# Kernel tuning notes

Measured on AMD Instinct MI355X. Metric: run time of the kernel, lower is better.

The kernel has to match this reference:

```python
import jax, jax.numpy as jnp
import numpy as np

N = 30000       # nodes
E = 480000      # edges (before self loops)
IN = 128        # in_channels
H1, C1 = 5, 64  # conv1 heads, per-head channels
OUT = 64        # out_channels (conv2, heads=1)
PE = 100000     # pos/neg edges for decode
NEG_SLOPE = 0.2


def setup_inputs() -> dict:
    key = jax.random.key(0)
    ks = jax.random.split(key, 12)
    return {
        "x": jax.random.normal(ks[0], (N, IN), dtype=jnp.float32),
        "edge_index": jax.random.randint(ks[1], (2, E), 0, N),
        "pos_edge_index": jax.random.randint(ks[2], (2, PE), 0, N),
        "neg_edge_index": jax.random.randint(ks[3], (2, PE), 0, N),
        "W1": jax.random.normal(ks[4], (IN, H1 * C1), dtype=jnp.float32) * 0.05,
        "att_src1": jax.random.normal(ks[5], (H1, C1), dtype=jnp.float32) * 0.1,
        "att_dst1": jax.random.normal(ks[6], (H1, C1), dtype=jnp.float32) * 0.1,
        "b1": jnp.zeros((H1 * C1,), dtype=jnp.float32),
        "W2": jax.random.normal(ks[7], (H1 * C1, OUT), dtype=jnp.float32) * 0.05,
        "att_src2": jax.random.normal(ks[8], (1, OUT), dtype=jnp.float32) * 0.1,
        "att_dst2": jax.random.normal(ks[9], (1, OUT), dtype=jnp.float32) * 0.1,
        "b2": jnp.zeros((OUT,), dtype=jnp.float32),
    }


def gat_conv(x, edge_index, W, att_src, att_dst, bias, heads, out_ch):
    """PyG GATConv: add self loops, linear proj, edge softmax, scatter-sum, concat heads."""
    n = x.shape[0]
    loops = jnp.arange(n)
    src = jnp.concatenate([edge_index[0], loops])  # message sources j
    dst = jnp.concatenate([edge_index[1], loops])  # message targets i
    h = (x @ W).reshape(n, heads, out_ch)          # [N,H,C]
    a_src = jnp.sum(h * att_src, axis=-1)          # [N,H]
    a_dst = jnp.sum(h * att_dst, axis=-1)          # [N,H]
    e = jax.nn.leaky_relu(a_src[src] + a_dst[dst], NEG_SLOPE)  # [E',H]
    # numerically-stable segment softmax over incoming edges of each dst node
    m = jax.ops.segment_max(e, dst, num_segments=n)
    m = jax.lax.stop_gradient(jnp.where(jnp.isfinite(m), m, 0.0))
    ex = jnp.exp(e - m[dst])
    s = jax.ops.segment_sum(ex, dst, num_segments=n)
    alpha = ex / (s[dst] + 1e-16)                  # [E',H]
    out = jax.ops.segment_sum(alpha[:, :, None] * h[src], dst, num_segments=n)  # [N,H,C]
    return out.reshape(n, heads * out_ch) + bias


def reference(x, edge_index, pos_edge_index, neg_edge_index,
              W1, att_src1, att_dst1, b1, W2, att_src2, att_dst2, b2):
    z = gat_conv(x, edge_index, W1, att_src1, att_dst1, b1, H1, C1)
    z = jax.nn.relu(z)
    z = gat_conv(z, edge_index, W2, att_src2, att_dst2, b2, 1, OUT)
    ei = jnp.concatenate([pos_edge_index, neg_edge_index], axis=-1)
    return jnp.sum(z[ei[0]] * z[ei[1]], axis=-1)  # [2*PE]
```

## Files before the change

### kernel.cpp

```cpp
#include <hip/hip_runtime.h>
#include <hip/hip_fp16.h>
#include <cstdint>
#include <cstddef>
#include <type_traits>

#define N_NODES 30000
#define N_EDGES 480000
#define N_EDGES_SL (N_EDGES + N_NODES)
#define IN_CH 128
#define HEADS1 5
#define C1 64
#define D1 (HEADS1 * C1)
#define OUT_CH 64
#define PE_CNT 100000
#define NEG_SLOPE 0.2f
#define BCAP 64
#define GEMM1_BLOCKS 469
#define INIT_BLOCKS 120
#define BB 120
#define EPB (N_EDGES / BB)
#define NW (N_NODES / 2)
#define PFX_BLOCKS 59
#define OVF_CAP 65536

typedef _Float16 f16x8 __attribute__((ext_vector_type(8)));
typedef _Float16 f16x2 __attribute__((ext_vector_type(2)));
typedef float fx4 __attribute__((ext_vector_type(4)));

#if defined(__has_builtin)
#if __has_builtin(__builtin_amdgcn_fdot2)
#define HAS_FDOT2 1
#endif
#endif

static __device__ __forceinline__ float leaky(float x) {
    return fmaxf(x, NEG_SLOPE * x);
}

template<int NH, int SP, typename AT>
static __device__ __forceinline__ void gemm_phase(const AT* __restrict__ A,
                                                  const __half* __restrict__ Wt,
                                                  __half* __restrict__ C, int K,
                                                  const float* __restrict__ att_src,
                                                  const float* __restrict__ att_dst,
                                                  float* __restrict__ as_out,
                                                  float* __restrict__ ad_out,
                                                  int slot, int nsl, int lane) {
    const int N = NH * 64;
    int q = lane >> 4, l16 = lane & 15;
    for (int tile = slot; tile < N_NODES / 16; tile += nsl) {
        int rowBase = tile * 16;
        int arow = rowBase + l16;
        fx4 zero4 = {0.f, 0.f, 0.f, 0.f};
        fx4 acc[NH][4];
#pragma unroll
        for (int h = 0; h < NH; ++h)
#pragma unroll
            for (int c = 0; c < 4; ++c) acc[h][c] = zero4;
        for (int kk = 0; kk < K; kk += 32) {
            f16x8 af;
            if constexpr (std::is_same<AT, float>::value) {
                const float4* s = (const float4*)(A + (size_t)arow * K + kk + q * 8);
                float4 v0 = s[0], v1 = s[1];
                af[0] = (_Float16)v0.x; af[1] = (_Float16)v0.y;
                af[2] = (_Float16)v0.z; af[3] = (_Float16)v0.w;
                af[4] = (_Float16)v1.x; af[5] = (_Float16)v1.y;
                af[6] = (_Float16)v1.z; af[7] = (_Float16)v1.w;
            } else {
                af = *(const f16x8*)((const __half*)A + (size_t)arow * K + kk + q * 8);
            }
#pragma unroll
            for (int h = 0; h < NH; ++h) {
#pragma unroll
                for (int c = 0; c < 4; ++c) {
                    int col = h * 64 + c * 16 + l16;
                    f16x8 bf = *(const f16x8*)(Wt + (size_t)col * K + kk + q * 8);
                    acc[h][c] = __builtin_amdgcn_mfma_f32_16x16x32_f16(af, bf, acc[h][c], 0, 0, 0);
                }
            }
        }
#pragma unroll
        for (int h = 0; h < NH; ++h) {
            float ps[4] = {0.f, 0.f, 0.f, 0.f};
            float pd[4] = {0.f, 0.f, 0.f, 0.f};
#pragma unroll
            for (int c = 0; c < 4; ++c) {
                int gcol = h * 64 + c * 16 + l16;
                float av = att_src[gcol];
                float dv = att_dst[gcol];
#pragma unroll
                for (int reg = 0; reg < 4; ++reg) {
                    int grow = rowBase + q * 4 + reg;
                    float val = acc[h][c][reg];
                    C[(size_t)grow * N + gcol] = __float2half(val);
                    ps[reg] += val * av;
                    pd[reg] += val * dv;
                }
            }
#pragma unroll
            for (int off = 1; off < 16; off <<= 1) {
#pragma unroll
                for (int reg = 0; reg < 4; ++reg) {
                    ps[reg] += __shfl_xor(ps[reg], off, 64);
                    pd[reg] += __shfl_xor(pd[reg], off, 64);
                }
            }
            if (l16 == 0) {
#pragma unroll
                for (int reg = 0; reg < 4; ++reg) {
                    int grow = rowBase + q * 4 + reg;
                    as_out[(size_t)grow * SP + h] = ps[reg];
                    ad_out[(size_t)grow * SP + h] = pd[reg];
                }
            }
        }
    }
}

__global__ __launch_bounds__(512) void k_init(int* __restrict__ ovfc,
                                              int* __restrict__ esrc2,
                                              const float* __restrict__ W1,
                                              __half* __restrict__ Wt1,
                                              const float* __restrict__ W2,
                                              __half* __restrict__ Wt2,
                                              const int* __restrict__ edge,
                                              unsigned* __restrict__ partA) {
    __shared__ unsigned bins[NW];
    if (blockIdx.x < INIT_BLOCKS) {
        int t = blockIdx.x * 512 + threadIdx.x;
        int nthr = INIT_BLOCKS * 512;
        for (int i = t; i < N_NODES; i += nthr) esrc2[i * BCAP] = i;
        if (t == 0) *ovfc = 0;
        const int T1 = IN_CH * D1, T2 = D1 * OUT_CH;
        for (int idx = t; idx < T1 + T2; idx += nthr) {
            if (idx < T1) {
                int k = idx / D1, n = idx - k * D1;
                Wt1[(size_t)n * IN_CH + k] = __float2half(W1[idx]);
            } else {
                int i2 = idx - T1;
                int k = i2 / OUT_CH, n = i2 - k * OUT_CH;
                Wt2[(size_t)n * D1 + k] = __float2half(W2[i2]);
            }
        }
    } else {
        int b = blockIdx.x - INIT_BLOCKS;
        for (int i = threadIdx.x; i < NW; i += 512) bins[i] = 0;
        __syncthreads();
        int e0 = b * EPB;
        for (int e = e0 + ((int)threadIdx.x << 2); e < e0 + EPB; e += 2048) {
            int4 dd = *(const int4*)(edge + N_EDGES + e);
            atomicAdd(&bins[dd.x >> 1], (dd.x & 1) ? 65536u : 1u);
            atomicAdd(&bins[dd.y >> 1], (dd.y & 1) ? 65536u : 1u);
            atomicAdd(&bins[dd.z >> 1], (dd.z & 1) ? 65536u : 1u);
            atomicAdd(&bins[dd.w >> 1], (dd.w & 1) ? 65536u : 1u);
        }
        __syncthreads();
        for (int i = threadIdx.x; i < NW; i += 512)
            partA[(size_t)b * NW + i] = bins[i];
    }
}

__global__ __launch_bounds__(256) void k_build_gemm1(const unsigned* __restrict__ partA,
                                                     unsigned* __restrict__ offA,
                                                     int* __restrict__ cnt,
                                                     const float* __restrict__ x,
                                                     const __half* __restrict__ Wt1,
                                                     __half* __restrict__ h1,
                                                     const float* __restrict__ att_src1,
                                                     const float* __restrict__ att_dst1,
                                                     float* __restrict__ as1,
                                                     float* __restrict__ ad1) {
    int lane = threadIdx.x & 63, wv = threadIdx.x >> 6;
    if (blockIdx.x < GEMM1_BLOCKS) {
        gemm_phase<HEADS1, 8, float>(x, Wt1, h1, IN_CH, att_src1, att_dst1, as1, ad1,
                                     blockIdx.x * 4 + wv, GEMM1_BLOCKS * 4, lane);
    } else {
        int w = (blockIdx.x - GEMM1_BLOCKS) * 256 + threadIdx.x;
        if (w < NW) {
            unsigned s0 = 1, s1 = 1;
            for (int b0 = 0; b0 < BB; b0 += 10) {
                unsigned v[10];
#pragma unroll
                for (int u = 0; u < 10; ++u)
                    v[u] = partA[(size_t)(b0 + u) * NW + w];
#pragma unroll
                for (int u = 0; u < 10; ++u) {
                    offA[(size_t)(b0 + u) * NW + w] = min(s0, 64u) | (min(s1, 64u) << 16);
                    s0 += v[u] & 0xFFFFu;
                    s1 += v[u] >> 16;
                }
            }
            cnt[2 * w] = (int)s0;
            cnt[2 * w + 1] = (int)s1;
        }
    }
}

__global__ __launch_bounds__(512) void k_rank(const int* __restrict__ edge,
                                              const unsigned* __restrict__ offA,
                                              int* __restrict__ esrc2,
                                              int* __restrict__ ovf_cnt,
                                              int* __restrict__ ovf) {
    __shared__ unsigned bins[NW];
    int b = blockIdx.x;
    for (int i = threadIdx.x; i < NW; i += 512) bins[i] = 0;
    __syncthreads();
    int e0 = b * EPB;
    for (int e = e0 + ((int)threadIdx.x << 2); e < e0 + EPB; e += 2048) {
        int4 dd = *(const int4*)(edge + N_EDGES + e);
        int4 ss = *(const int4*)(edge + e);
        int dv[4] = {dd.x, dd.y, dd.z, dd.w};
        int sv[4] = {ss.x, ss.y, ss.z, ss.w};
#pragma unroll
        for (int u = 0; u < 4; ++u) {
            int d = dv[u];
            unsigned ret = atomicAdd(&bins[d >> 1], (d & 1) ? 65536u : 1u);
            unsigned lr = (d & 1) ? (ret >> 16) : (ret & 0xFFFFu);
            unsigned off = offA[(size_t)b * NW + (d >> 1)];
            off = (d & 1) ? (off >> 16) : (off & 0xFFFFu);
            unsigned slot = off + lr;
            if (slot < BCAP) {
                esrc2[(d << 6) + slot] = sv[u];
            } else {
                int oi = atomicAdd(ovf_cnt, 1);
                if (oi < OVF_CAP) { ovf[2 * oi] = d; ovf[2 * oi + 1] = sv[u]; }
            }
        }
    }
}

template<int NH, int NS, bool RELU>
static __device__ __forceinline__ void gather_all(const __half* __restrict__ base,
                                                  const unsigned (&wpkw)[NH][64],
                                                  const int (&jbufw)[64],
                                                  float (&redw)[584],
                                                  const float* __restrict__ bias,
                                                  __half* __restrict__ zrow,
                                                  int es, int cg, int lane) {
    int kA = es, kB = es + 8, kC = es + 16, kD = es + 24;
    int jA = jbufw[kA], jB = jbufw[kB];
    int jC = (NS == 4) ? jbufw[kC] : 0;
    int jD = (NS == 4) ? jbufw[kD] : 0;
    float4 v[NH][4];
#pragma unroll
    for (int h = 0; h < NH; ++h) {
        const __half* hb = base + h * 64;
        v[h][0] = *(const float4*)(hb + jA);
        v[h][1] = *(const float4*)(hb + jB);
        if (NS == 4) {
            v[h][2] = *(const float4*)(hb + jC);
            v[h][3] = *(const float4*)(hb + jD);
        }
    }
#pragma unroll
    for (int h = 0; h < NH; ++h) {
        unsigned uA = wpkw[h][kA], uB = wpkw[h][kB];
        __half2 hwA = *(__half2*)&uA, hwB = *(__half2*)&uB;
        const __half2* pA = (const __half2*)&v[h][0];
        const __half2* pB = (const __half2*)&v[h][1];
        __half2 a2[4] = {__half2{0, 0}, __half2{0, 0}, __half2{0, 0}, __half2{0, 0}};
#pragma unroll
        for (int i = 0; i < 4; ++i) {
            a2[i] = __hfma2(pA[i], hwA, a2[i]);
            a2[i] = __hfma2(pB[i], hwB, a2[i]);
        }
        if (NS == 4) {
            unsigned uC = wpkw[h][kC], uD = wpkw[h][kD];
            __half2 hwC = *(__half2*)&uC, hwD = *(__half2*)&uD;
            const __half2* pC = (const __half2*)&v[h][2];
            const __half2* pD = (const __half2*)&v[h][3];
#pragma unroll
            for (int i = 0; i < 4; ++i) {
                a2[i] = __hfma2(pC[i], hwC, a2[i]);
                a2[i] = __hfma2(pD[i], hwD, a2[i]);
            }
        }
#pragma unroll
        for (int i = 0; i < 4; ++i) {
            float2 f = __half22float2(a2[i]);
            redw[(cg * 8 + 2 * i) * 9 + es] = f.x;
            redw[(cg * 8 + 2 * i + 1) * 9 + es] = f.y;
        }
        float tot = 0.f;
#pragma unroll
        for (int e2 = 0; e2 < 8; ++e2)
            tot += redw[lane * 9 + e2];
        float o = tot + bias[h * 64 + lane];
        if (RELU) o = fmaxf(o, 0.f);
        zrow[h * 64 + lane] = __float2half(o);
    }
}

template<int NH, bool RELU>
__global__ __launch_bounds__(256) void k_attn_agg(const int* __restrict__ cnt,
                                                  const int* __restrict__ esrc2,
                                                  const int* __restrict__ ovf_cnt,
                                                  const int* __restrict__ ovf,
                                                  const __half* __restrict__ hf,
                                                  const float* __restrict__ a_src,
                                                  const float* __restrict__ a_dst,
                                                  const float* __restrict__ bias,
                                                  __half* __restrict__ zout) {
    const int SP = (NH == 1) ? 1 : 8;
    __shared__ unsigned wpk[4][NH][64];
    __shared__ int jbuf[4][64];
    __shared__ float red[4][584];
    int node = (blockIdx.x * 256 + threadIdx.x) >> 6;
    int lane = threadIdx.x & 63;
    int wv = threadIdx.x >> 6;
    if (node >= N_NODES) return;
    int deg = cnt[node];
    const int RS = NH * 64;
    float da[NH];
    if constexpr (NH == 1) {
        da[0] = a_dst[node];
    } else {
        float4 d0 = *(const float4*)(a_dst + (size_t)node * SP);
        da[0] = d0.x; da[1] = d0.y; da[2] = d0.z; da[3] = d0.w;
        da[4] = a_dst[(size_t)node * SP + 4];
    }
    if (deg <= BCAP) {
        int es = lane >> 3, cg = lane & 7;
        int joff = 0;
        float e[NH];
#pragma unroll
        for (int h = 0; h < NH; ++h) e[h] = 0.f;
        if (lane < deg) {
            int j = esrc2[node * BCAP + lane];
            joff = j * RS;
            if constexpr (NH == 1) {
                e[0] = __expf(leaky(a_src[j] + da[0]));
            } else {
                float4 s0 = *(const float4*)(a_src + (size_t)j * SP);
                float s4 = a_src[(size_t)j * SP + 4];
                e[0] = __expf(leaky(s0.x + da[0]));
                e[1] = __expf(leaky(s0.y + da[1]));
                e[2] = __expf(leaky(s0.z + da[2]));
                e[3] = __expf(leaky(s0.w + da[3]));
                e[4] = __expf(leaky(s4 + da[4]));
            }
        }
        float s[NH];
#pragma unroll
        for (int h = 0; h < NH; ++h) s[h] = e[h];
#pragma unroll
        for (int off = 1; off < 64; off <<= 1) {
#pragma unroll
            for (int h = 0; h < NH; ++h) s[h] += __shfl_xor(s[h], off, 64);
        }
#pragma unroll
        for (int h = 0; h < NH; ++h) {
            float r = 1.f / (s[h] + 1e-16f);
            __half2 wn = __float2half2_rn(e[h] * r);
            wpk[wv][h][lane] = *(unsigned*)&wn;
        }
        jbuf[wv][lane] = joff;
        const __half* base = hf + cg * 8;
        __half* zrow = zout + (size_t)node * RS;
        if (deg <= 16) {
            gather_all<NH, 2, RELU>(base, wpk[wv], jbuf[wv], red[wv], bias, zrow, es, cg, lane);
        } else if (deg <= 32) {
            gather_all<NH, 4, RELU>(base, wpk[wv], jbuf[wv], red[wv], bias, zrow, es, cg, lane);
        } else {
#pragma unroll
            for (int h = 0; h < NH; ++h) {
                const __half* hbase = hf + h * 64 + cg * 8;
                __half2 acch[4] = {__half2{0, 0}, __half2{0, 0}, __half2{0, 0}, __half2{0, 0}};
                for (int k0 = 0; k0 < deg; k0 += 32) {
                    int kA = k0 + es, kB = kA + 8, kC = kA + 16, kD = kA + 24;
                    unsigned uA = wpk[wv][h][kA];
                    unsigned uB = wpk[wv][h][kB];
                    unsigned uC = wpk[wv][h][kC];
                    unsigned uD = wpk[wv][h][kD];
                    int jA = jbuf[wv][kA];
                    int jB = jbuf[wv][kB];
                    int jC = jbuf[wv][kC];
                    int jD = jbuf[wv][kD];
                    float4 vA = *(const float4*)(hbase + jA);
                    float4 vB = *(const float4*)(hbase + jB);
                    float4 vC = *(const float4*)(hbase + jC);
                    float4 vD = *(const float4*)(hbase + jD);
                    __half2 hwA = *(__half2*)&uA, hwB = *(__half2*)&uB;
                    __half2 hwC = *(__half2*)&uC, hwD = *(__half2*)&uD;
                    const __half2* pA = (const __half2*)&vA;
                    const __half2* pB = (const __half2*)&vB;
                    const __half2* pC = (const __half2*)&vC;
                    const __half2* pD = (const __half2*)&vD;
#pragma unroll
                    for (int i = 0; i < 4; ++i) {
                        acch[i] = __hfma2(pA[i], hwA, acch[i]);
                        acch[i] = __hfma2(pB[i], hwB, acch[i]);
                        acch[i] = __hfma2(pC[i], hwC, acch[i]);
                        acch[i] = __hfma2(pD[i], hwD, acch[i]);
                    }
                }
#pragma unroll
                for (int i = 0; i < 4; ++i) {
                    float2 f = __half22float2(acch[i]);
                    red[wv][(cg * 8 + 2 * i) * 9 + es] = f.x;
                    red[wv][(cg * 8 + 2 * i + 1) * 9 + es] = f.y;
                }
                float tot = 0.f;
#pragma unroll
                for (int e2 = 0; e2 < 8; ++e2)
                    tot += red[wv][lane * 9 + e2];
                float o = tot + bias[h * 64 + lane];
                if (RELU) o = fmaxf(o, 0.f);
                zrow[h * 64 + lane] = __float2half(o);
            }
        }
    } else {
        int ovn = min(*ovf_cnt, OVF_CAP);
#pragma unroll
        for (int h = 0; h < NH; ++h) {
            float adsth = da[h];
            float sden = __expf(leaky(a_src[(size_t)esrc2[node * BCAP + lane] * SP + h] + adsth));
#pragma unroll
            for (int off = 1; off < 64; off <<= 1)
                sden += __shfl_xor(sden, off, 64);
            float s2 = 0.f;
            for (int k = lane; k < ovn; k += 64)
                if (ovf[2 * k] == node)
                    s2 += __expf(leaky(a_src[(size_t)ovf[2 * k + 1] * SP + h] + adsth));
#pragma unroll
            for (int off = 1; off < 64; off <<= 1)
                s2 += __shfl_xor(s2, off, 64);
            float r = 1.f / (sden + s2 + 1e-16f);
            float a = 0.f;
            for (int k = 0; k < BCAP; ++k) {
                int j = esrc2[node * BCAP + k];
                float w = __expf(leaky(a_src[(size_t)j * SP + h] + adsth));
                a += w * __half2float(hf[(size_t)j * RS + h * 64 + lane]);
            }
            for (int k = 0; k < ovn; ++k) {
                if (ovf[2 * k] == node) {
                    int j = ovf[2 * k + 1];
                    float w = __expf(leaky(a_src[(size_t)j * SP + h] + adsth));
                    a += w * __half2float(hf[(size_t)j * RS + h * 64 + lane]);
                }
            }
            float o = a * r + bias[h * 64 + lane];
            if (RELU) o = fmaxf(o, 0.f);
            zout[(size_t)node * RS + h * 64 + lane] = __float2half(o);
        }
    }
}

__global__ __launch_bounds__(256) void k_gemm2(const __half* __restrict__ z1,
                                               const __half* __restrict__ Wt2,
                                               __half* __restrict__ h2,
                                               const float* __restrict__ att_src2,
                                               const float* __restrict__ att_dst2,
                                               float* __restrict__ as2,
                                               float* __restrict__ ad2) {
    int lane = threadIdx.x & 63, wv = threadIdx.x >> 6;
    gemm_phase<1, 1, __half>(z1, Wt2, h2, D1, att_src2, att_dst2, as2, ad2,
                             blockIdx.x * 4 + wv, gridDim.x * 4, lane);
}

__global__ __launch_bounds__(256) void k_decode(const int* __restrict__ pos,
                                                const int* __restrict__ neg,
                                                const __half* __restrict__ z2,
                                                float* __restrict__ out) {
    int t = blockIdx.x * 256 + threadIdx.x;
    int e = t >> 3;
    int lc = t & 7;
    if (e >= 2 * PE_CNT) return;
    int a, b;
    if (e < PE_CNT) { a = pos[e]; b = pos[PE_CNT + e]; }
    else { int k = e - PE_CNT; a = neg[k]; b = neg[PE_CNT + k]; }
    union U { float4 f; f16x2 h[4]; __half2 hh[4]; } ua, ub;
    ua.f = *(const float4*)(z2 + (size_t)a * OUT_CH + lc * 8);
    ub.f = *(const float4*)(z2 + (size_t)b * OUT_CH + lc * 8);
    float v = 0.f;
#pragma unroll
    for (int i = 0; i < 4; ++i) {
#ifdef HAS_FDOT2
        v = __builtin_amdgcn_fdot2(ua.h[i], ub.h[i], v, false);
#else
        float2 fa = __half22float2(ua.hh[i]);
        float2 fb = __half22float2(ub.hh[i]);
        v += fa.x * fb.x + fa.y * fb.y;
#endif
    }
#pragma unroll
    for (int off = 1; off < 8; off <<= 1)
        v += __shfl_xor(v, off, 64);
    if (lc == 0) out[e] = v;
}

extern "C" void kernel_launch(void* const* d_in, const int* in_sizes, int n_in,
                              void* d_out, int out_size, void* d_ws, size_t ws_size,
                              hipStream_t stream) {
    const float* x        = (const float*)d_in[0];
    const int* edge_index = (const int*)d_in[1];
    const int* pos_ei     = (const int*)d_in[2];
    const int* neg_ei     = (const int*)d_in[3];
    const float* W1       = (const float*)d_in[4];
    const float* att_src1 = (const float*)d_in[5];
    const float* att_dst1 = (const float*)d_in[6];
    const float* b1       = (const float*)d_in[7];
    const float* W2       = (const float*)d_in[8];
    const float* att_src2 = (const float*)d_in[9];
    const float* att_dst2 = (const float*)d_in[10];
    const float* b2       = (const float*)d_in[11];
    float* out            = (float*)d_out;

    char* ws = (char*)d_ws;
    size_t off = 0;
    auto alloc = [&](size_t bytes) -> void* {
        void* p = ws + off;
        off = (off + bytes + 255) & ~(size_t)255;
        return p;
    };
    int* cnt     = (int*)alloc(sizeof(int) * N_NODES);
    int* ovfc    = (int*)alloc(sizeof(int) * 8);
    int* esrc2   = (int*)alloc(sizeof(int) * (size_t)N_NODES * BCAP);
    int* ovf     = (int*)alloc(sizeof(int) * (size_t)2 * OVF_CAP);
    __half* h1   = (__half*)alloc(sizeof(__half) * (size_t)N_NODES * D1);
    __half* z1   = (__half*)alloc(sizeof(__half) * (size_t)N_NODES * D1);
    __half* h2   = (__half*)alloc(sizeof(__half) * (size_t)N_NODES * OUT_CH);
    __half* z2   = (__half*)alloc(sizeof(__half) * (size_t)N_NODES * OUT_CH);
    __half* Wt1  = (__half*)alloc(sizeof(__half) * (size_t)D1 * IN_CH);
    __half* Wt2  = (__half*)alloc(sizeof(__half) * (size_t)OUT_CH * D1);
    float* as1   = (float*)alloc(sizeof(float) * (size_t)N_NODES * 8);
    float* ad1   = (float*)alloc(sizeof(float) * (size_t)N_NODES * 8);
    float* as2   = (float*)alloc(sizeof(float) * (size_t)N_NODES);
    float* ad2   = (float*)alloc(sizeof(float) * (size_t)N_NODES);
    unsigned* partA = (unsigned*)z1;
    unsigned* offA  = (unsigned*)((char*)z1 + (size_t)BB * NW * sizeof(unsigned));

    k_init<<<INIT_BLOCKS + BB, 512, 0, stream>>>(ovfc, esrc2, W1, Wt1, W2, Wt2,
                                                 edge_index, partA);
    k_build_gemm1<<<GEMM1_BLOCKS + PFX_BLOCKS, 256, 0, stream>>>(
        partA, offA, cnt, x, Wt1, h1, att_src1, att_dst1, as1, ad1);
    k_rank<<<BB, 512, 0, stream>>>(edge_index, offA, esrc2, ovfc, ovf);
    k_attn_agg<HEADS1, true><<<(N_NODES + 3) / 4, 256, 0, stream>>>(
        cnt, esrc2, ovfc, ovf, h1, as1, ad1, b1, z1);
    k_gemm2<<<469, 256, 0, stream>>>(z1, Wt2, h2, att_src2, att_dst2, as2, ad2);
    k_attn_agg<1, false><<<(N_NODES + 3) / 4, 256, 0, stream>>>(
        cnt, esrc2, ovfc, ovf, h2, as2, ad2, b2, z2);
    k_decode<<<(2 * PE_CNT * 8 + 255) / 256, 256, 0, stream>>>(pos_ei, neg_ei, z2, out);

    (void)in_sizes; (void)n_in; (void)out_size; (void)ws_size;
}
```

Measured before the change: 205.3 us.

## Fold attention projections into GEMM weights as extra MFMA column group

Precomputes W·att_src and W·att_dst as extra weight columns appended to the transposed fp16 weight matrices, so each GEMM computes the attention logits a_src/a_dst with one additional 16-column MFMA tile instead of a post-GEMM dot product plus cross-lane shuffle reduction. This removes the epilogue reductions and shuffles in both GEMMs. It also adds a launch bound hint of 2 waves-per-EU occupancy on the aggregation kernel. The logits are now computed from fp16-rounded folded weights, which changes numerics slightly.

```diff
diff --git a/kernel.cpp b/kernel.cpp
--- a/kernel.cpp
+++ b/kernel.cpp
@@ -11,7 +11,9 @@
 #define HEADS1 5
 #define C1 64
 #define D1 (HEADS1 * C1)
+#define D1X (D1 + 16)
 #define OUT_CH 64
+#define OUT_CHX (OUT_CH + 16)
 #define PE_CNT 100000
 #define NEG_SLOPE 0.2f
 #define BCAP 64
@@ -41,22 +43,19 @@
 static __device__ __forceinline__ void gemm_phase(const AT* __restrict__ A,
                                                   const __half* __restrict__ Wt,
                                                   __half* __restrict__ C, int K,
-                                                  const float* __restrict__ att_src,
-                                                  const float* __restrict__ att_dst,
                                                   float* __restrict__ as_out,
                                                   float* __restrict__ ad_out,
                                                   int slot, int nsl, int lane) {
     const int N = NH * 64;
+    const int NCG = NH * 4 + 1;
     int q = lane >> 4, l16 = lane & 15;
     for (int tile = slot; tile < N_NODES / 16; tile += nsl) {
         int rowBase = tile * 16;
         int arow = rowBase + l16;
         fx4 zero4 = {0.f, 0.f, 0.f, 0.f};
-        fx4 acc[NH][4];
-#pragma unroll
-        for (int h = 0; h < NH; ++h)
-#pragma unroll
-            for (int c = 0; c < 4; ++c) acc[h][c] = zero4;
+        fx4 acc[NCG];
+#pragma unroll
+        for (int g = 0; g < NCG; ++g) acc[g] = zero4;
         for (int kk = 0; kk < K; kk += 32) {
             f16x8 af;
             if constexpr (std::is_same<AT, float>::value) {
@@ -70,48 +69,31 @@
                 af = *(const f16x8*)((const __half*)A + (size_t)arow * K + kk + q * 8);
             }
 #pragma unroll
-            for (int h = 0; h < NH; ++h) {
-#pragma unroll
-                for (int c = 0; c < 4; ++c) {
-                    int col = h * 64 + c * 16 + l16;
-                    f16x8 bf = *(const f16x8*)(Wt + (size_t)col * K + kk + q * 8);
-                    acc[h][c] = __builtin_amdgcn_mfma_f32_16x16x32_f16(af, bf, acc[h][c], 0, 0, 0);
-                }
-            }
-        }
-#pragma unroll
-        for (int h = 0; h < NH; ++h) {
-            float ps[4] = {0.f, 0.f, 0.f, 0.f};
-            float pd[4] = {0.f, 0.f, 0.f, 0.f};
-#pragma unroll
-            for (int c = 0; c < 4; ++c) {
-                int gcol = h * 64 + c * 16 + l16;
-                float av = att_src[gcol];
-                float dv = att_dst[gcol];
-#pragma unroll
-                for (int reg = 0; reg < 4; ++reg) {
-                    int grow = rowBase + q * 4 + reg;
-                    float val = acc[h][c][reg];
-                    C[(size_t)grow * N + gcol] = __float2half(val);
-                    ps[reg] += val * av;
-                    pd[reg] += val * dv;
-                }
-            }
-#pragma unroll
-            for (int off = 1; off < 16; off <<= 1) {
-#pragma unroll
-                for (int reg = 0; reg < 4; ++reg) {
-                    ps[reg] += __shfl_xor(ps[reg], off, 64);
-                    pd[reg] += __shfl_xor(pd[reg], off, 64);
-                }
-            }
-            if (l16 == 0) {
-#pragma unroll
-                for (int reg = 0; reg < 4; ++reg) {
-                    int grow = rowBase + q * 4 + reg;
-                    as_out[(size_t)grow * SP + h] = ps[reg];
-                    ad_out[(size_t)grow * SP + h] = pd[reg];
-                }
+            for (int g = 0; g < NCG; ++g) {
+                int col = g * 16 + l16;
+                f16x8 bf = *(const f16x8*)(Wt + (size_t)col * K + kk + q * 8);
+                acc[g] = __builtin_amdgcn_mfma_f32_16x16x32_f16(af, bf, acc[g], 0, 0, 0);
+            }
+        }
+#pragma unroll
+        for (int g = 0; g < NH * 4; ++g) {
+            int gcol = g * 16 + l16;
+#pragma unroll
+            for (int reg = 0; reg < 4; ++reg) {
+                int grow = rowBase + q * 4 + reg;
+                C[(size_t)grow * N + gcol] = __float2half(acc[g][reg]);
+            }
+        }
+#pragma unroll
+        for (int reg = 0; reg < 4; ++reg) {
+            int grow = rowBase + q * 4 + reg;
+            float val = acc[NH * 4][reg];
+            if constexpr (SP == 8) {
+                if (l16 < HEADS1) as_out[(size_t)grow * 8 + l16] = val;
+                else if (l16 >= 8 && l16 < 8 + HEADS1) ad_out[(size_t)grow * 8 + (l16 - 8)] = val;
+            } else {
+                if (l16 == 0) as_out[grow] = val;
+                else if (l16 == 8) ad_out[grow] = val;
             }
         }
     }
@@ -120,9 +102,13 @@
 __global__ __launch_bounds__(512) void k_init(int* __restrict__ ovfc,
                                               int* __restrict__ esrc2,
                                               const float* __restrict__ W1,
-                                              __half* __restrict__ Wt1,
+                                              __half* __restrict__ Wt1x,
                                               const float* __restrict__ W2,
-                                              __half* __restrict__ Wt2,
+                                              __half* __restrict__ Wt2x,
+                                              const float* __restrict__ att_src1,
+                                              const float* __restrict__ att_dst1,
+                                              const float* __restrict__ att_src2,
+                                              const float* __restrict__ att_dst2,
                                               const int* __restrict__ edge,
                                               unsigned* __restrict__ partA) {
     __shared__ unsigned bins[NW];
@@ -135,12 +121,43 @@
         for (int idx = t; idx < T1 + T2; idx += nthr) {
             if (idx < T1) {
                 int k = idx / D1, n = idx - k * D1;
-                Wt1[(size_t)n * IN_CH + k] = __float2half(W1[idx]);
+                Wt1x[(size_t)n * IN_CH + k] = __float2half(W1[idx]);
             } else {
                 int i2 = idx - T1;
                 int k = i2 / OUT_CH, n = i2 - k * OUT_CH;
-                Wt2[(size_t)n * D1 + k] = __float2half(W2[i2]);
-            }
+                Wt2x[(size_t)n * D1 + k] = __float2half(W2[i2]);
+            }
+        }
+        for (int i = t; i < 1280; i += nthr) {
+            int k = i / 10, v = i - k * 10;
+            int h = (v >= 5) ? v - 5 : v;
+            const float* att = (v >= 5) ? att_dst1 : att_src1;
+            float a = 0.f;
+#pragma unroll 8
+            for (int c = 0; c < 64; ++c)
+                a += W1[(size_t)k * D1 + h * 64 + c] * att[h * 64 + c];
+            int col = D1 + ((v >= 5) ? 8 : 0) + h;
+            Wt1x[(size_t)col * IN_CH + k] = __float2half(a);
+        }
+        for (int i = t; i < 768; i += nthr) {
+            int c6 = i >> 7, k = i & 127;
+            int col = (c6 < 3) ? (D1 + 5 + c6) : (D1 + 10 + c6);
+            Wt1x[(size_t)col * IN_CH + k] = __half(0);
+        }
+        for (int i = t; i < 640; i += nthr) {
+            int k = i >> 1, v = i & 1;
+            const float* att = v ? att_dst2 : att_src2;
+            float a = 0.f;
+#pragma unroll 8
+            for (int c = 0; c < 64; ++c)
+                a += W2[(size_t)k * OUT_CH + c] * att[c];
+            int col = OUT_CH + v * 8;
+            Wt2x[(size_t)col * D1 + k] = __float2half(a);
+        }
+        for (int i = t; i < 4480; i += nthr) {
+            int c14 = i / 320, k = i - c14 * 320;
+            int col = (c14 < 7) ? (OUT_CH + 1 + c14) : (OUT_CH + 2 + c14);
+            Wt2x[(size_t)col * D1 + k] = __half(0);
         }
     } else {
         int b = blockIdx.x - INIT_BLOCKS;
@@ -164,15 +181,13 @@
                                                      unsigned* __restrict__ offA,
                                                      int* __restrict__ cnt,
                                                      const float* __restrict__ x,
-                                                     const __half* __restrict__ Wt1,
+                                                     const __half* __restrict__ Wt1x,
                                                      __half* __restrict__ h1,
-                                                     const float* __restrict__ att_src1,
-                                                     const float* __restrict__ att_dst1,
                                                      float* __restrict__ as1,
                                                      float* __restrict__ ad1) {
     int lane = threadIdx.x & 63, wv = threadIdx.x >> 6;
     if (blockIdx.x < GEMM1_BLOCKS) {
-        gemm_phase<HEADS1, 8, float>(x, Wt1, h1, IN_CH, att_src1, att_dst1, as1, ad1,
+        gemm_phase<HEADS1, 8, float>(x, Wt1x, h1, IN_CH, as1, ad1,
                                      blockIdx.x * 4 + wv, GEMM1_BLOCKS * 4, lane);
     } else {
         int w = (blockIdx.x - GEMM1_BLOCKS) * 256 + threadIdx.x;
@@ -292,7 +307,7 @@
 }
 
 template<int NH, bool RELU>
-__global__ __launch_bounds__(256) void k_attn_agg(const int* __restrict__ cnt,
+__global__ __launch_bounds__(256, 2) void k_attn_agg(const int* __restrict__ cnt,
                                                   const int* __restrict__ esrc2,
                                                   const int* __restrict__ ovf_cnt,
                                                   const int* __restrict__ ovf,
@@ -447,14 +462,12 @@
 }
 
 __global__ __launch_bounds__(256) void k_gemm2(const __half* __restrict__ z1,
-                                               const __half* __restrict__ Wt2,
+                                               const __half* __restrict__ Wt2x,
                                                __half* __restrict__ h2,
-                                               const float* __restrict__ att_src2,
-                                               const float* __restrict__ att_dst2,
                                                float* __restrict__ as2,
                                                float* __restrict__ ad2) {
     int lane = threadIdx.x & 63, wv = threadIdx.x >> 6;
-    gemm_phase<1, 1, __half>(z1, Wt2, h2, D1, att_src2, att_dst2, as2, ad2,
+    gemm_phase<1, 1, __half>(z1, Wt2x, h2, D1, as2, ad2,
                              blockIdx.x * 4 + wv, gridDim.x * 4, lane);
 }
 
@@ -521,8 +534,8 @@
     __half* z1   = (__half*)alloc(sizeof(__half) * (size_t)N_NODES * D1);
     __half* h2   = (__half*)alloc(sizeof(__half) * (size_t)N_NODES * OUT_CH);
     __half* z2   = (__half*)alloc(sizeof(__half) * (size_t)N_NODES * OUT_CH);
-    __half* Wt1  = (__half*)alloc(sizeof(__half) * (size_t)D1 * IN_CH);
-    __half* Wt2  = (__half*)alloc(sizeof(__half) * (size_t)OUT_CH * D1);
+    __half* Wt1x = (__half*)alloc(sizeof(__half) * (size_t)D1X * IN_CH);
+    __half* Wt2x = (__half*)alloc(sizeof(__half) * (size_t)OUT_CHX * D1);
     float* as1   = (float*)alloc(sizeof(float) * (size_t)N_NODES * 8);
     float* ad1   = (float*)alloc(sizeof(float) * (size_t)N_NODES * 8);
     float* as2   = (float*)alloc(sizeof(float) * (size_t)N_NODES);
@@ -530,14 +543,15 @@
     unsigned* partA = (unsigned*)z1;
     unsigned* offA  = (unsigned*)((char*)z1 + (size_t)BB * NW * sizeof(unsigned));
 
-    k_init<<<INIT_BLOCKS + BB, 512, 0, stream>>>(ovfc, esrc2, W1, Wt1, W2, Wt2,
+    k_init<<<INIT_BLOCKS + BB, 512, 0, stream>>>(ovfc, esrc2, W1, Wt1x, W2, Wt2x,
+                                                 att_src1, att_dst1, att_src2, att_dst2,
                                                  edge_index, partA);
     k_build_gemm1<<<GEMM1_BLOCKS + PFX_BLOCKS, 256, 0, stream>>>(
-        partA, offA, cnt, x, Wt1, h1, att_src1, att_dst1, as1, ad1);
+        partA, offA, cnt, x, Wt1x, h1, as1, ad1);
     k_rank<<<BB, 512, 0, stream>>>(edge_index, offA, esrc2, ovfc, ovf);
     k_attn_agg<HEADS1, true><<<(N_NODES + 3) / 4, 256, 0, stream>>>(
         cnt, esrc2, ovfc, ovf, h1, as1, ad1, b1, z1);
-    k_gemm2<<<469, 256, 0, stream>>>(z1, Wt2, h2, att_src2, att_dst2, as2, ad2);
+    k_gemm2<<<469, 256, 0, stream>>>(z1, Wt2x, h2, as2, ad2);
     k_attn_agg<1, false><<<(N_NODES + 3) / 4, 256, 0, stream>>>(
         cnt, esrc2, ovfc, ovf, h2, as2, ad2, b2, z2);
     k_decode<<<(2 * PE_CNT * 8 + 255) / 256, 256, 0, stream>>>(pos_ei, neg_ei, z2, out);
```

Result: slower. 217.5 us (+6.0%).

## Fold attention vectors into weights and compute scores via separate MFMA blocks

Applied to the files above, without the earlier changes.

Precomputes W·att_src and W·att_dst as small extra fp16 weight columns during init. Extra blocks then compute the per-node attention scores with one MFMA tile, instead of reducing them with shuffles in the GEMM epilogue. This drops the epilogue reductions and score writes from the main GEMM blocks at the cost of re-reading the input activations. It also halves the number of edge-binning blocks (BB from 120 to 60), and the scores now carry fp16 rounding of the folded weights.

```diff
diff --git a/kernel.cpp b/kernel.cpp
--- a/kernel.cpp
+++ b/kernel.cpp
@@ -6,7 +6,6 @@
 
 #define N_NODES 30000
 #define N_EDGES 480000
-#define N_EDGES_SL (N_EDGES + N_NODES)
 #define IN_CH 128
 #define HEADS1 5
 #define C1 64
@@ -16,8 +15,11 @@
 #define NEG_SLOPE 0.2f
 #define BCAP 64
 #define GEMM1_BLOCKS 469
+#define GEMM2_BLOCKS 469
+#define SG1_BLOCKS 64
+#define SG2_BLOCKS 64
 #define INIT_BLOCKS 120
-#define BB 120
+#define BB 60
 #define EPB (N_EDGES / BB)
 #define NW (N_NODES / 2)
 #define PFX_BLOCKS 59
@@ -37,14 +39,10 @@
     return fmaxf(x, NEG_SLOPE * x);
 }
 
-template<int NH, int SP, typename AT>
+template<int NH, typename AT>
 static __device__ __forceinline__ void gemm_phase(const AT* __restrict__ A,
                                                   const __half* __restrict__ Wt,
                                                   __half* __restrict__ C, int K,
-                                                  const float* __restrict__ att_src,
-                                                  const float* __restrict__ att_dst,
-                                                  float* __restrict__ as_out,
-                                                  float* __restrict__ ad_out,
                                                   int slot, int nsl, int lane) {
     const int N = NH * 64;
     int q = lane >> 4, l16 = lane & 15;
@@ -81,37 +79,55 @@
         }
 #pragma unroll
         for (int h = 0; h < NH; ++h) {
-            float ps[4] = {0.f, 0.f, 0.f, 0.f};
-            float pd[4] = {0.f, 0.f, 0.f, 0.f};
 #pragma unroll
             for (int c = 0; c < 4; ++c) {
                 int gcol = h * 64 + c * 16 + l16;
-                float av = att_src[gcol];
-                float dv = att_dst[gcol];
 #pragma unroll
                 for (int reg = 0; reg < 4; ++reg) {
                     int grow = rowBase + q * 4 + reg;
-                    float val = acc[h][c][reg];
-                    C[(size_t)grow * N + gcol] = __float2half(val);
-                    ps[reg] += val * av;
-                    pd[reg] += val * dv;
+                    C[(size_t)grow * N + gcol] = __float2half(acc[h][c][reg]);
                 }
             }
-#pragma unroll
-            for (int off = 1; off < 16; off <<= 1) {
-#pragma unroll
-                for (int reg = 0; reg < 4; ++reg) {
-                    ps[reg] += __shfl_xor(ps[reg], off, 64);
-                    pd[reg] += __shfl_xor(pd[reg], off, 64);
-                }
-            }
-            if (l16 == 0) {
-#pragma unroll
-                for (int reg = 0; reg < 4; ++reg) {
-                    int grow = rowBase + q * 4 + reg;
-                    as_out[(size_t)grow * SP + h] = ps[reg];
-                    ad_out[(size_t)grow * SP + h] = pd[reg];
-                }
+        }
+    }
+}
+
+template<int SP, typename AT>
+static __device__ __forceinline__ void score_gemm(const AT* __restrict__ A,
+                                                  const __half* __restrict__ Wta,
+                                                  int K,
+                                                  float* __restrict__ as_out,
+                                                  float* __restrict__ ad_out,
+                                                  int slot, int nsl, int lane) {
+    int q = lane >> 4, l16 = lane & 15;
+    for (int tile = slot; tile < N_NODES / 16; tile += nsl) {
+        int rowBase = tile * 16;
+        int arow = rowBase + l16;
+        fx4 acc = {0.f, 0.f, 0.f, 0.f};
+        for (int kk = 0; kk < K; kk += 32) {
+            f16x8 af;
+            if constexpr (std::is_same<AT, float>::value) {
+                const float4* s = (const float4*)(A + (size_t)arow * K + kk + q * 8);
+                float4 v0 = s[0], v1 = s[1];
+                af[0] = (_Float16)v0.x; af[1] = (_Float16)v0.y;
+                af[2] = (_Float16)v0.z; af[3] = (_Float16)v0.w;
+                af[4] = (_Float16)v1.x; af[5] = (_Float16)v1.y;
+                af[6] = (_Float16)v1.z; af[7] = (_Float16)v1.w;
+            } else {
+                af = *(const f16x8*)((const __half*)A + (size_t)arow * K + kk + q * 8);
+            }
+            f16x8 bf = *(const f16x8*)(Wta + (size_t)l16 * K + kk + q * 8);
+            acc = __builtin_amdgcn_mfma_f32_16x16x32_f16(af, bf, acc, 0, 0, 0);
+        }
+#pragma unroll
+        for (int reg = 0; reg < 4; ++reg) {
+            int grow = rowBase + q * 4 + reg;
+            if constexpr (SP == 8) {
+                if (l16 < HEADS1) as_out[(size_t)grow * 8 + l16] = acc[reg];
+                else if (l16 >= 8 && l16 < 8 + HEADS1) ad_out[(size_t)grow * 8 + (l16 - 8)] = acc[reg];
+            } else {
+                if (l16 == 0) as_out[grow] = acc[reg];
+                else if (l16 == 8) ad_out[grow] = acc[reg];
             }
         }
     }
@@ -123,6 +139,12 @@
                                               __half* __restrict__ Wt1,
                                               const float* __restrict__ W2,
                                               __half* __restrict__ Wt2,
+                                              __half* __restrict__ Wt1a,
+                                              __half* __restrict__ Wt2a,
+                                              const float* __restrict__ att_src1,
+                                              const float* __restrict__ att_dst1,
+                                              const float* __restrict__ att_src2,
+                                              const float* __restrict__ att_dst2,
                                               const int* __restrict__ edge,
                                               unsigned* __restrict__ partA) {
     __shared__ unsigned bins[NW];
@@ -142,6 +164,37 @@
                 Wt2[(size_t)n * D1 + k] = __float2half(W2[i2]);
             }
         }
+        for (int i = t; i < 1280; i += nthr) {
+            int k = i / 10, v = i - k * 10;
+            int h = (v >= 5) ? v - 5 : v;
+            const float* att = (v >= 5) ? att_dst1 : att_src1;
+            float a = 0.f;
+#pragma unroll 8
+            for (int c = 0; c < 64; ++c)
+                a += W1[(size_t)k * D1 + h * 64 + c] * att[h * 64 + c];
+            int col = ((v >= 5) ? 8 : 0) + h;
+            Wt1a[(size_t)col * IN_CH + k] = __float2half(a);
+        }
+        for (int i = t; i < 768; i += nthr) {
+            int c6 = i >> 7, k = i & 127;
+            int col = (c6 < 3) ? (5 + c6) : (10 + c6);
+            Wt1a[(size_t)col * IN_CH + k] = __half(0);
+        }
+        for (int i = t; i < 640; i += nthr) {
+            int k = i >> 1, v = i & 1;
+            const float* att = v ? att_dst2 : att_src2;
+            float a = 0.f;
+#pragma unroll 8
+            for (int c = 0; c < 64; ++c)
+                a += W2[(size_t)k * OUT_CH + c] * att[c];
+            int col = v * 8;
+            Wt2a[(size_t)col * D1 + k] = __float2half(a);
+        }
+        for (int i = t; i < 4480; i += nthr) {
+            int c14 = i / 320, k = i - c14 * 320;
+            int col = (c14 < 7) ? (1 + c14) : (2 + c14);
+            Wt2a[(size_t)col * D1 + k] = __half(0);
+        }
     } else {
         int b = blockIdx.x - INIT_BLOCKS;
         for (int i = threadIdx.x; i < NW; i += 512) bins[i] = 0;
@@ -165,16 +218,15 @@
                                                      int* __restrict__ cnt,
                                                      const float* __restrict__ x,
                                                      const __half* __restrict__ Wt1,
+                                                     const __half* __restrict__ Wt1a,
                                                      __half* __restrict__ h1,
-                                                     const float* __restrict__ att_src1,
-                                                     const float* __restrict__ att_dst1,
                                                      float* __restrict__ as1,
                                                      float* __restrict__ ad1) {
     int lane = threadIdx.x & 63, wv = threadIdx.x >> 6;
     if (blockIdx.x < GEMM1_BLOCKS) {
-        gemm_phase<HEADS1, 8, float>(x, Wt1, h1, IN_CH, att_src1, att_dst1, as1, ad1,
-                                     blockIdx.x * 4 + wv, GEMM1_BLOCKS * 4, lane);
-    } else {
+        gemm_phase<HEADS1, float>(x, Wt1, h1, IN_CH,
+                                  blockIdx.x * 4 + wv, GEMM1_BLOCKS * 4, lane);
+    } else if (blockIdx.x < GEMM1_BLOCKS + PFX_BLOCKS) {
         int w = (blockIdx.x - GEMM1_BLOCKS) * 256 + threadIdx.x;
         if (w < NW) {
             unsigned s0 = 1, s1 = 1;
@@ -193,6 +245,10 @@
             cnt[2 * w] = (int)s0;
             cnt[2 * w + 1] = (int)s1;
         }
+    } else {
+        int sb = blockIdx.x - GEMM1_BLOCKS - PFX_BLOCKS;
+        score_gemm<8, float>(x, Wt1a, IN_CH, as1, ad1,
+                             sb * 4 + wv, SG1_BLOCKS * 4, lane);
     }
 }
 
@@ -448,14 +504,19 @@
 
 __global__ __launch_bounds__(256) void k_gemm2(const __half* __restrict__ z1,
                                                const __half* __restrict__ Wt2,
+                                               const __half* __restrict__ Wt2a,
                                                __half* __restrict__ h2,
-                                               const float* __restrict__ att_src2,
-                                               const float* __restrict__ att_dst2,
                                                float* __restrict__ as2,
                                                float* __restrict__ ad2) {
     int lane = threadIdx.x & 63, wv = threadIdx.x >> 6;
-    gemm_phase<1, 1, __half>(z1, Wt2, h2, D1, att_src2, att_dst2, as2, ad2,
-                             blockIdx.x * 4 + wv, gridDim.x * 4, lane);
+    if (blockIdx.x < GEMM2_BLOCKS) {
+        gemm_phase<1, __half>(z1, Wt2, h2, D1,
+                              blockIdx.x * 4 + wv, GEMM2_BLOCKS * 4, lane);
+    } else {
+        int sb = blockIdx.x - GEMM2_BLOCKS;
+        score_gemm<1, __half>(z1, Wt2a, D1, as2, ad2,
+                              sb * 4 + wv, SG2_BLOCKS * 4, lane);
+    }
 }
 
 __global__ __launch_bounds__(256) void k_decode(const int* __restrict__ pos,
@@ -523,6 +584,8 @@
     __half* z2   = (__half*)alloc(sizeof(__half) * (size_t)N_NODES * OUT_CH);
     __half* Wt1  = (__half*)alloc(sizeof(__half) * (size_t)D1 * IN_CH);
     __half* Wt2  = (__half*)alloc(sizeof(__half) * (size_t)OUT_CH * D1);
+    __half* Wt1a = (__half*)alloc(sizeof(__half) * (size_t)16 * IN_CH);
+    __half* Wt2a = (__half*)alloc(sizeof(__half) * (size_t)16 * D1);
     float* as1   = (float*)alloc(sizeof(float) * (size_t)N_NODES * 8);
     float* ad1   = (float*)alloc(sizeof(float) * (size_t)N_NODES * 8);
     float* as2   = (float*)alloc(sizeof(float) * (size_t)N_NODES);
@@ -531,13 +594,15 @@
     unsigned* offA  = (unsigned*)((char*)z1 + (size_t)BB * NW * sizeof(unsigned));
 
     k_init<<<INIT_BLOCKS + BB, 512, 0, stream>>>(ovfc, esrc2, W1, Wt1, W2, Wt2,
+                                                 Wt1a, Wt2a,
+                                                 att_src1, att_dst1, att_src2, att_dst2,
                                                  edge_index, partA);
-    k_build_gemm1<<<GEMM1_BLOCKS + PFX_BLOCKS, 256, 0, stream>>>(
-        partA, offA, cnt, x, Wt1, h1, att_src1, att_dst1, as1, ad1);
+    k_build_gemm1<<<GEMM1_BLOCKS + PFX_BLOCKS + SG1_BLOCKS, 256, 0, stream>>>(
+        partA, offA, cnt, x, Wt1, Wt1a, h1, as1, ad1);
     k_rank<<<BB, 512, 0, stream>>>(edge_index, offA, esrc2, ovfc, ovf);
     k_attn_agg<HEADS1, true><<<(N_NODES + 3) / 4, 256, 0, stream>>>(
         cnt, esrc2, ovfc, ovf, h1, as1, ad1, b1, z1);
-    k_gemm2<<<469, 256, 0, stream>>>(z1, Wt2, h2, att_src2, att_dst2, as2, ad2);
+    k_gemm2<<<GEMM2_BLOCKS + SG2_BLOCKS, 256, 0, stream>>>(z1, Wt2, Wt2a, h2, as2, ad2);
     k_attn_agg<1, false><<<(N_NODES + 3) / 4, 256, 0, stream>>>(
         cnt, esrc2, ovfc, ovf, h2, as2, ad2, b2, z2);
     k_decode<<<(2 * PE_CNT * 8 + 255) / 256, 256, 0, stream>>>(pos_ei, neg_ei, z2, out);
```

Measured after the change: 234.1 us. 14.0% more time.
